# Performance work log

Hardware: AMD Instinct MI355X
Metric: run time of the kernel (lower is better)

Reference implementation:

```python
import jax, jax.numpy as jnp
import numpy as np

B, S, DM, H, DK, DH = 8, 1024, 512, 8, 32, 64
LN_EPS = 1e-5
NEG_SLOPE = 0.01  # torch LeakyReLU default


def _l2norm(t, axis=-1, eps=1e-12):
    # matches F.normalize(p=2): x / max(||x||, eps)
    n = jnp.sqrt(jnp.sum(t * t, axis=axis, keepdims=True))
    return t / jnp.maximum(n, eps)


def _layernorm(t, w, b, eps=LN_EPS):
    mu = jnp.mean(t, axis=-1, keepdims=True)
    var = jnp.mean((t - mu) ** 2, axis=-1, keepdims=True)
    return (t - mu) * jax.lax.rsqrt(var + eps) * w + b


def setup_inputs() -> dict:
    key = jax.random.key(0)
    ks = jax.random.split(key, 16)
    x = jax.random.normal(ks[0], (B, S, DM), dtype=jnp.float32)
    # causal-style mask: True = masked (upper triangle)
    attn_mask = jnp.broadcast_to(jnp.triu(jnp.ones((S, S), dtype=bool), k=1), (B, S, S))
    pairwise_dist = jax.random.uniform(ks[1], (B, S, S), dtype=jnp.float32)
    s = 0.02
    return {
        "x": x,
        "attn_mask": attn_mask,
        "pairwise_dist": pairwise_dist,
        "Wq": jax.random.normal(ks[2], (H, DK, DM), dtype=jnp.float32) * s,
        "Wk": jax.random.normal(ks[3], (H, DK, DM), dtype=jnp.float32) * s,
        "Wv": jax.random.normal(ks[4], (H, DH, DM), dtype=jnp.float32) * s,
        "omega": jnp.ones((H,), dtype=jnp.float32),
        "Wo": jax.random.normal(ks[5], (DM, H * DH), dtype=jnp.float32) * s,
        "bo": jnp.zeros((DM,), dtype=jnp.float32),
        "Wf": jax.random.normal(ks[6], (DM, DM), dtype=jnp.float32) * s,
        "bf": jnp.zeros((DM,), dtype=jnp.float32),
        "ln1_w": jnp.ones((DM,), dtype=jnp.float32),
        "ln1_b": jnp.zeros((DM,), dtype=jnp.float32),
        "ln2_w": jnp.ones((DM,), dtype=jnp.float32),
        "ln2_b": jnp.zeros((DM,), dtype=jnp.float32),
    }


def _encoder_layer(x, attn_mask, pairwise_dist, Wq, Wk, Wv, omega,
                   Wo, bo, Wf, bf, ln1_w, ln1_b, ln2_w, ln2_b):
    # --- multi-head self-attention, all heads batched ---
    q = _l2norm(jnp.einsum('bsd,hkd->hbsk', x, Wq))   # [H,B,S,DK]
    k = _l2norm(jnp.einsum('bsd,hkd->hbsk', x, Wk))
    v = jnp.einsum('bsd,hvd->hbsv', x, Wv)            # [H,B,S,DH]
    scores = jnp.einsum('hbsk,hbtk->hbst', q, k)      # cosine-sim, [H,B,S,S]
    # distance bias: exp(-omega*d) - 1, detached in the original
    r = jax.lax.stop_gradient(
        jnp.exp(-omega[:, None, None, None] * pairwise_dist[None]) - 1.0)
    scores = scores + r
    scores = jnp.where(attn_mask[None], -jnp.inf, scores)
    # custom softmax: exp(x) / (sum + 1); exp(-inf)=0 handles masking
    z = jnp.exp(scores)
    attn = z / (jnp.sum(z, axis=-1, keepdims=True) + 1.0)
    y = jnp.einsum('hbst,hbtv->hbsv', attn, v)        # [H,B,S,DH]
    y = jnp.transpose(y, (1, 2, 0, 3)).reshape(x.shape[0], x.shape[1], -1)  # concat heads
    x_attn = y @ Wo.T + bo
    # --- residual + LN + FFN (dropout p=0 -> identity) ---
    z1 = _layernorm(x + x_attn, ln1_w, ln1_b)
    z_ff = jax.nn.leaky_relu(z1 @ Wf.T + bf, negative_slope=NEG_SLOPE)
    return _layernorm(z1 + z_ff, ln2_w, ln2_b)


def reference(x, attn_mask, pairwise_dist, Wq, Wk, Wv, omega,
              Wo, bo, Wf, bf, ln1_w, ln1_b, ln2_w, ln2_b):
    return _encoder_layer(x, attn_mask, pairwise_dist, Wq, Wk, Wv, omega,
                          Wo, bo, Wf, bf, ln1_w, ln1_b, ln2_w, ln2_b)
```

## Files before the change

kernel.cpp:

```cpp
#include <hip/hip_runtime.h>
#include <hip/hip_bf16.h>
#include <math.h>
#include <stdint.h>

#define BB 8
#define SS 1024
#define DMM 512
#define HH 8
#define DKK 32
#define DHH 64

typedef __bf16 bf16x8 __attribute__((ext_vector_type(8)));
typedef float f32x4 __attribute__((ext_vector_type(4)));

__device__ __forceinline__ void gll16(const void* g, void* l) {
  __builtin_amdgcn_global_load_lds(
      (const __attribute__((address_space(1))) void*)(uintptr_t)g,
      (__attribute__((address_space(3))) void*)(uint32_t)(uintptr_t)l,
      16, 0, 0);
}

__device__ __forceinline__ uint4 pack8(const float4 a, const float4 b) {
  union { __hip_bfloat162 h2[4]; uint4 u; } p;
  p.h2[0] = __float22bfloat162_rn(make_float2(a.x, a.y));
  p.h2[1] = __float22bfloat162_rn(make_float2(a.z, a.w));
  p.h2[2] = __float22bfloat162_rn(make_float2(b.x, b.y));
  p.h2[3] = __float22bfloat162_rn(make_float2(b.z, b.w));
  return p.u;
}

__device__ __constant__ unsigned char dJ[24]  = {15,15,14,7,14,13,13,12,6,12,11,11,10,5,10,9,9,8,4,8,3,2,1,0};
__device__ __constant__ unsigned char dTB[24] = {0,8,0,0,8,0,7,0,0,7,0,6,0,0,6,0,5,0,0,5,0,0,0,0};
__device__ __constant__ unsigned char dTE[24] = {8,16,8,8,15,7,14,7,7,13,6,12,6,6,11,5,10,5,5,9,4,3,2,1};

__global__ __launch_bounds__(256) void cvt_all(
    const float* __restrict__ x, const float* __restrict__ Wq,
    const float* __restrict__ Wk, const float* __restrict__ Wv,
    const float* __restrict__ Wo, const float* __restrict__ Wf,
    __bf16* __restrict__ xb, __bf16* __restrict__ Wcat,
    __bf16* __restrict__ Wob, __bf16* __restrict__ Wfb) {
  size_t i = ((size_t)blockIdx.x * 256 + threadIdx.x) * 8;
  const float* s;
  __bf16* d;
  size_t off;
  if (i < 4194304) { s = x; d = xb + i; off = i; }
  else {
    size_t j = i - 4194304;
    if (j < 524288) {
      d = Wcat + j;
      if (j < 131072) { s = Wq; off = j; }
      else if (j < 262144) { s = Wk; off = j - 131072; }
      else { s = Wv; off = j - 262144; }
    } else {
      size_t jj = j - 524288;
      if (jj < 262144) { s = Wo; d = Wob + jj; off = jj; }
      else { s = Wf; d = Wfb + (jj - 262144); off = jj - 262144; }
    }
  }
  float4 a = *(const float4*)&s[off];
  float4 b = *(const float4*)&s[off + 4];
  *(uint4*)d = pack8(a, b);
}

__global__ __launch_bounds__(256) void gemm_qkv(
    const __bf16* __restrict__ A, const __bf16* __restrict__ W,
    __bf16* __restrict__ Qg, __bf16* __restrict__ Kg,
    __bf16* __restrict__ Vrow) {
  __shared__ __bf16 As[2][128 * 32];
  __shared__ __bf16 Bs[2][128 * 32];
  const int tid = threadIdx.x;
  const int n0 = blockIdx.x * 128;
  const int m0 = blockIdx.y * 128;
  const int lane = tid & 63;
  const int w = tid >> 6;
  const int wm = (w & 1) * 64, wn = (w >> 1) * 64;
  const int fr = lane & 15, quad = lane >> 4;
  const int srow = lane >> 2;
  const int schunk = (lane & 3) ^ ((lane >> 3) & 3);

  f32x4 acc[4][4];
#pragma unroll
  for (int mi = 0; mi < 4; ++mi)
#pragma unroll
    for (int ni = 0; ni < 4; ++ni) acc[mi][ni] = (f32x4){0.f, 0.f, 0.f, 0.f};

#pragma unroll
  for (int j = 0; j < 2; ++j) {
    const int seg = w * 2 + j;
    const int row = seg * 16 + srow;
    gll16(&A[(size_t)(m0 + row) * 512 + schunk * 8], &As[0][seg * 512]);
    gll16(&W[(size_t)(n0 + row) * 512 + schunk * 8], &Bs[0][seg * 512]);
  }
  for (int it = 0; it < 16; ++it) {
    __syncthreads();
    if (it < 15) {
      const int kt = (it + 1) * 32, ib = (it + 1) & 1;
#pragma unroll
      for (int j = 0; j < 2; ++j) {
        const int seg = w * 2 + j;
        const int row = seg * 16 + srow;
        gll16(&A[(size_t)(m0 + row) * 512 + kt + schunk * 8], &As[ib][seg * 512]);
        gll16(&W[(size_t)(n0 + row) * 512 + kt + schunk * 8], &Bs[ib][seg * 512]);
      }
    }
    const __bf16* as = As[it & 1];
    const __bf16* bs = Bs[it & 1];
    bf16x8 af[4], bfv[4];
    const int rsw = (quad ^ ((fr >> 1) & 3)) * 8;
#pragma unroll
    for (int mi = 0; mi < 4; ++mi)
      af[mi] = *(const bf16x8*)&as[(wm + mi * 16 + fr) * 32 + rsw];
#pragma unroll
    for (int ni = 0; ni < 4; ++ni)
      bfv[ni] = *(const bf16x8*)&bs[(wn + ni * 16 + fr) * 32 + rsw];
#pragma unroll
    for (int mi = 0; mi < 4; ++mi)
#pragma unroll
      for (int ni = 0; ni < 4; ++ni)
        acc[mi][ni] = __builtin_amdgcn_mfma_f32_16x16x32_bf16(
            af[mi], bfv[ni], acc[mi][ni], 0, 0, 0);
  }

  const int er = quad * 4;
  const int ec = fr;
  if (n0 < 512) {
    const bool isq = (n0 < 256);
    __bf16* G = isq ? Qg : Kg;
    const int nb = isq ? n0 : n0 - 256;
#pragma unroll
    for (int mi = 0; mi < 4; ++mi) {
#pragma unroll
      for (int p = 0; p < 2; ++p) {
        const int hh = (nb + wn + p * 32) >> 5;
#pragma unroll
        for (int r = 0; r < 4; ++r) {
          float v0 = acc[mi][2 * p][r], v1 = acc[mi][2 * p + 1][r];
          float ss = v0 * v0 + v1 * v1;
          ss += __shfl_xor(ss, 1, 64);
          ss += __shfl_xor(ss, 2, 64);
          ss += __shfl_xor(ss, 4, 64);
          ss += __shfl_xor(ss, 8, 64);
          const float sc = 1.0f / fmaxf(sqrtf(ss), 1e-12f);
          const int mm = m0 + wm + mi * 16 + er + r;
          const int bb = mm >> 10, s = mm & 1023;
          __bf16* gp = G + ((size_t)(bb * 8 + hh) * 1024 + s) * 32;
          gp[ec] = (__bf16)(v0 * sc);
          gp[16 + ec] = (__bf16)(v1 * sc);
        }
      }
    }
  } else {
#pragma unroll
    for (int mi = 0; mi < 4; ++mi)
#pragma unroll
      for (int ni = 0; ni < 4; ++ni) {
        const int n = n0 - 512 + wn + ni * 16 + ec;
#pragma unroll
        for (int r = 0; r < 4; ++r) {
          const int mm = m0 + wm + mi * 16 + er + r;
          Vrow[(size_t)mm * 512 + n] = (__bf16)acc[mi][ni][r];
        }
      }
  }
}

template <int MODE>
__global__ __launch_bounds__(256) void gemm_bf16(
    const __bf16* __restrict__ A, const __bf16* __restrict__ W,
    const float* __restrict__ bias, const float* __restrict__ resid,
    float* __restrict__ C, int N) {
  __shared__ __bf16 As[2][128 * 32];
  __shared__ __bf16 Bs[2][128 * 32];
  const int tid = threadIdx.x;
  const int n0 = blockIdx.x * 128;
  const int m0 = blockIdx.y * 128;
  const int lane = tid & 63;
  const int w = tid >> 6;
  const int wm = (w & 1) * 64, wn = (w >> 1) * 64;
  const int fr = lane & 15, quad = lane >> 4;
  const int srow = lane >> 2;
  const int schunk = (lane & 3) ^ ((lane >> 3) & 3);

  f32x4 acc[4][4];
#pragma unroll
  for (int mi = 0; mi < 4; ++mi)
#pragma unroll
    for (int ni = 0; ni < 4; ++ni) acc[mi][ni] = (f32x4){0.f, 0.f, 0.f, 0.f};

#pragma unroll
  for (int j = 0; j < 2; ++j) {
    const int seg = w * 2 + j;
    const int row = seg * 16 + srow;
    gll16(&A[(size_t)(m0 + row) * 512 + schunk * 8], &As[0][seg * 512]);
    gll16(&W[(size_t)(n0 + row) * 512 + schunk * 8], &Bs[0][seg * 512]);
  }
  for (int it = 0; it < 16; ++it) {
    __syncthreads();
    if (it < 15) {
      const int kt = (it + 1) * 32, ib = (it + 1) & 1;
#pragma unroll
      for (int j = 0; j < 2; ++j) {
        const int seg = w * 2 + j;
        const int row = seg * 16 + srow;
        gll16(&A[(size_t)(m0 + row) * 512 + kt + schunk * 8], &As[ib][seg * 512]);
        gll16(&W[(size_t)(n0 + row) * 512 + kt + schunk * 8], &Bs[ib][seg * 512]);
      }
    }
    const __bf16* as = As[it & 1];
    const __bf16* bs = Bs[it & 1];
    bf16x8 af[4], bfv[4];
    const int rsw = (quad ^ ((fr >> 1) & 3)) * 8;
#pragma unroll
    for (int mi = 0; mi < 4; ++mi)
      af[mi] = *(const bf16x8*)&as[(wm + mi * 16 + fr) * 32 + rsw];
#pragma unroll
    for (int ni = 0; ni < 4; ++ni)
      bfv[ni] = *(const bf16x8*)&bs[(wn + ni * 16 + fr) * 32 + rsw];
#pragma unroll
    for (int mi = 0; mi < 4; ++mi)
#pragma unroll
      for (int ni = 0; ni < 4; ++ni)
        acc[mi][ni] = __builtin_amdgcn_mfma_f32_16x16x32_bf16(
            af[mi], bfv[ni], acc[mi][ni], 0, 0, 0);
  }

  const int er = quad * 4;
  const int ec = fr;
#pragma unroll
  for (int mi = 0; mi < 4; ++mi) {
#pragma unroll
    for (int ni = 0; ni < 4; ++ni) {
      const int n = n0 + wn + ni * 16 + ec;
      float bsv = bias[n];
#pragma unroll
      for (int r = 0; r < 4; ++r) {
        const int m = m0 + wm + mi * 16 + er + r;
        float v = acc[mi][ni][r];
        if (MODE == 1) {
          v += bsv + resid[(size_t)m * 512 + n];
        } else {
          float g = v + bsv;
          g = g > 0.f ? g : 0.01f * g;
          v = resid[(size_t)m * 512 + n] + g;
        }
        C[(size_t)m * N + n] = v;
      }
    }
  }
}

__global__ __launch_bounds__(256) void v_transpose(
    const __bf16* __restrict__ Vrow, __bf16* __restrict__ Vt) {
  __shared__ __bf16 vt[64][136];
  const int bh = blockIdx.x;
  const int b = bh >> 3, h = bh & 7;
  const int sb = blockIdx.y * 128;
  const int tid = threadIdx.x;
#pragma unroll
  for (int i = 0; i < 8; ++i) {
    int idx = tid + i * 256;
    int t = idx >> 4, vd4 = (idx & 15) * 4;
    union { uint2 u; __bf16 e[4]; } v;
    v.u = *(const uint2*)&Vrow[((size_t)(b * 1024 + sb + t)) * 512 + h * 64 + vd4];
    vt[vd4 + 0][t] = v.e[0];
    vt[vd4 + 1][t] = v.e[1];
    vt[vd4 + 2][t] = v.e[2];
    vt[vd4 + 3][t] = v.e[3];
  }
  __syncthreads();
  {
    const int vd = tid >> 2, tseg = (tid & 3) * 32;
    uint4* o = (uint4*)(Vt + (size_t)bh * 65536 + (size_t)vd * 1024 + sb + tseg);
#pragma unroll
    for (int j = 0; j < 4; ++j)
      o[j] = *(const uint4*)&vt[vd][tseg + j * 8];
  }
}

__global__ __launch_bounds__(256) void attn_fused(
    const __bf16* __restrict__ Qg, const __bf16* __restrict__ Kg,
    const __bf16* __restrict__ Vt, const float* __restrict__ dist,
    const float* __restrict__ omega, __bf16* __restrict__ y,
    float* __restrict__ Pacc, float* __restrict__ Zb) {
  __shared__ __bf16 Ks[64 * 32];
  __shared__ __bf16 Vs[64 * 64];
  __shared__ __bf16 zbuf[4][16][72];

  const int bh = blockIdx.x;
  const int entry = blockIdx.y;
  const int b = bh >> 3, h = bh & 7;
  const int jidx = dJ[entry];
  const int tbeg = dTB[entry];
  const int tend = dTE[entry];
  const int s0 = jidx * 64;
  const int tid = threadIdx.x;
  const int lane = tid & 63;
  const int w = tid >> 6;
  const int q = lane >> 4;
  const int m = lane & 15;
  const float om = omega[h];

  const int sl = s0 + w * 16 + m;
  const bf16x8 bq = *(const bf16x8*)&Qg[((size_t)bh * 1024 + sl) * 32 + q * 8];
  const int kswz = (q ^ ((m >> 1) & 3)) * 8;

  f32x4 acc[4];
#pragma unroll
  for (int ni = 0; ni < 4; ++ni) acc[ni] = (f32x4){0.f, 0.f, 0.f, 0.f};
  float zsum = 0.0f;

  for (int tt = tbeg; tt < tend; ++tt) {
    const int t0 = tt * 64;
    __syncthreads();
    {
      int row = tid >> 2, p = tid & 3;
      uint4 v = *(const uint4*)&Kg[((size_t)bh * 1024 + t0 + row) * 32 + p * 8];
      *(uint4*)&Ks[row * 32 + ((p ^ ((row >> 1) & 3)) * 8)] = v;
    }
#pragma unroll
    for (int i = 0; i < 2; ++i) {
      int idx = tid + i * 256;
      int vd = idx >> 3, p = idx & 7;
      uint4 v = *(const uint4*)&Vt[(size_t)bh * 65536 + (size_t)vd * 1024 + t0 + p * 8];
      *(uint4*)&Vs[vd * 64 + ((p ^ (vd & 7)) * 8)] = v;
    }
    float4 dv[4];
#pragma unroll
    for (int mi = 0; mi < 4; ++mi)
      dv[mi] = *(const float4*)&dist[((size_t)b * 1024 + sl) * 1024 + t0 + 16 * mi + q * 4];
    __syncthreads();

#pragma unroll
    for (int mi = 0; mi < 4; ++mi) {
      const bf16x8 ak = *(const bf16x8*)&Ks[(16 * mi + m) * 32 + kswz];
      f32x4 s4 = __builtin_amdgcn_mfma_f32_16x16x32_bf16(
          ak, bq, (f32x4){0.f, 0.f, 0.f, 0.f}, 0, 0, 0);
      float zr[4];
#pragma unroll
      for (int r = 0; r < 4; ++r) {
        const int t = t0 + 16 * mi + q * 4 + r;
        float zv = __expf(s4[r] + __expf(-om * (&dv[mi].x)[r]) - 1.0f);
        zr[r] = (t <= sl) ? zv : 0.0f;
        zsum += zr[r];
      }
      union { __hip_bfloat162 h2[2]; uint2 u; } pz;
      pz.h2[0] = __float22bfloat162_rn(make_float2(zr[0], zr[1]));
      pz.h2[1] = __float22bfloat162_rn(make_float2(zr[2], zr[3]));
      *(uint2*)&zbuf[w][m][16 * mi + q * 4] = pz.u;
    }
    const bf16x8 az0 = *(const bf16x8*)&zbuf[w][m][q * 8];
    const bf16x8 az1 = *(const bf16x8*)&zbuf[w][m][32 + q * 8];
#pragma unroll
    for (int ni = 0; ni < 4; ++ni) {
      const bf16x8 vb0 = *(const bf16x8*)&Vs[(16 * ni + m) * 64 + ((q ^ (m & 7)) * 8)];
      const bf16x8 vb1 = *(const bf16x8*)&Vs[(16 * ni + m) * 64 + (((q + 4) ^ (m & 7)) * 8)];
      acc[ni] = __builtin_amdgcn_mfma_f32_16x16x32_bf16(az0, vb0, acc[ni], 0, 0, 0);
      acc[ni] = __builtin_amdgcn_mfma_f32_16x16x32_bf16(az1, vb1, acc[ni], 0, 0, 0);
    }
  }

  zsum += __shfl_xor(zsum, 16, 64);
  zsum += __shfl_xor(zsum, 32, 64);

  if (jidx < 8) {
#pragma unroll
    for (int r = 0; r < 4; ++r) {
      const float dn = __shfl(zsum, q * 4 + r, 64);
      const float inv = 1.0f / (dn + 1.0f);
      __bf16* yp = &y[((size_t)b * 1024 + s0 + w * 16 + q * 4 + r) * 512 + h * 64 + m];
#pragma unroll
      for (int ni = 0; ni < 4; ++ni)
        yp[ni * 16] = (__bf16)(acc[ni][r] * inv);
    }
  } else {
    const int half = (tbeg != 0) ? 1 : 0;
    const size_t pidx = (size_t)((bh * 8 + (jidx - 8)) * 2 + half);
    float* Pp = Pacc + pidx * 4096;
    float* Zp = Zb + pidx * 64;
#pragma unroll
    for (int r = 0; r < 4; ++r) {
      const int row = w * 16 + q * 4 + r;
      const float dn = __shfl(zsum, q * 4 + r, 64);
      if (m == 0) Zp[row] = dn;
#pragma unroll
      for (int ni = 0; ni < 4; ++ni)
        Pp[row * 64 + ni * 16 + m] = acc[ni][r];
    }
  }
}

__global__ __launch_bounds__(256) void attn_reduce(
    const float* __restrict__ Pacc, const float* __restrict__ Zb,
    __bf16* __restrict__ y) {
  const int e = blockIdx.x;
  const int bh = e >> 3, j = (e & 7) + 8;
  const int b = bh >> 3, h = bh & 7;
  const float* p0 = Pacc + (size_t)e * 2 * 4096;
  const float* p1 = p0 + 4096;
  const int row = threadIdx.x >> 2;
  const int c0 = (threadIdx.x & 3) * 16;
  const float z = Zb[(size_t)e * 128 + row] + Zb[(size_t)e * 128 + 64 + row];
  const float inv = 1.0f / (z + 1.0f);
  float4 o[4];
#pragma unroll
  for (int i = 0; i < 4; ++i) {
    const float4 a = *(const float4*)&p0[row * 64 + c0 + i * 4];
    const float4 c = *(const float4*)&p1[row * 64 + c0 + i * 4];
    o[i].x = (a.x + c.x) * inv; o[i].y = (a.y + c.y) * inv;
    o[i].z = (a.z + c.z) * inv; o[i].w = (a.w + c.w) * inv;
  }
  __bf16* yp = &y[((size_t)b * 1024 + j * 64 + row) * 512 + h * 64 + c0];
  *(uint4*)yp = pack8(o[0], o[1]);
  *(uint4*)(yp + 8) = pack8(o[2], o[3]);
}

__global__ __launch_bounds__(256) void ln_kernel(
    const float* __restrict__ in, const float* __restrict__ w,
    const float* __restrict__ bvec, float* __restrict__ out,
    __bf16* __restrict__ outb) {
  const int row = blockIdx.x * 4 + (threadIdx.x >> 6);
  const int lane = threadIdx.x & 63;
  const float4* ip = (const float4*)(in + (size_t)row * 512);
  float4 a = ip[lane * 2], c = ip[lane * 2 + 1];
  float s = a.x + a.y + a.z + a.w + c.x + c.y + c.z + c.w;
#pragma unroll
  for (int off = 32; off > 0; off >>= 1) s += __shfl_xor(s, off, 64);
  const float mu = s * (1.0f / 512.0f);
  a.x -= mu; a.y -= mu; a.z -= mu; a.w -= mu;
  c.x -= mu; c.y -= mu; c.z -= mu; c.w -= mu;
  float s2 = a.x * a.x + a.y * a.y + a.z * a.z + a.w * a.w +
             c.x * c.x + c.y * c.y + c.z * c.z + c.w * c.w;
#pragma unroll
  for (int off = 32; off > 0; off >>= 1) s2 += __shfl_xor(s2, off, 64);
  const float inv = rsqrtf(s2 * (1.0f / 512.0f) + 1e-5f);
  const float4 w0 = ((const float4*)w)[lane * 2], w1 = ((const float4*)w)[lane * 2 + 1];
  const float4 b0 = ((const float4*)bvec)[lane * 2], b1 = ((const float4*)bvec)[lane * 2 + 1];
  float4 o0, o1;
  o0.x = a.x * inv * w0.x + b0.x; o0.y = a.y * inv * w0.y + b0.y;
  o0.z = a.z * inv * w0.z + b0.z; o0.w = a.w * inv * w0.w + b0.w;
  o1.x = c.x * inv * w1.x + b1.x; o1.y = c.y * inv * w1.y + b1.y;
  o1.z = c.z * inv * w1.z + b1.z; o1.w = c.w * inv * w1.w + b1.w;
  float4* op = (float4*)(out + (size_t)row * 512);
  op[lane * 2] = o0; op[lane * 2 + 1] = o1;
  if (outb) *(uint4*)&outb[(size_t)row * 512 + lane * 8] = pack8(o0, o1);
}

extern "C" void kernel_launch(void* const* d_in, const int* in_sizes, int n_in,
                              void* d_out, int out_size, void* d_ws, size_t ws_size,
                              hipStream_t stream) {
  const float* x = (const float*)d_in[0];
  const float* dist = (const float*)d_in[2];
  const float* Wq = (const float*)d_in[3];
  const float* Wk = (const float*)d_in[4];
  const float* Wv = (const float*)d_in[5];
  const float* omega = (const float*)d_in[6];
  const float* Wo = (const float*)d_in[7];
  const float* bo = (const float*)d_in[8];
  const float* Wf = (const float*)d_in[9];
  const float* bf_ = (const float*)d_in[10];
  const float* ln1w = (const float*)d_in[11];
  const float* ln1b = (const float*)d_in[12];
  const float* ln2w = (const float*)d_in[13];
  const float* ln2b = (const float*)d_in[14];
  float* out = (float*)d_out;

  char* base = (char*)d_ws;
  const size_t MB = 1 << 20;
  __bf16* xb = (__bf16*)base;
  __bf16* yb = (__bf16*)base;
  __bf16* Wcat = (__bf16*)(base + 8 * MB);
  __bf16* Wob = (__bf16*)(base + 9 * MB);
  __bf16* Wfb = (__bf16*)(base + 9 * MB + 512 * 1024);
  __bf16* Qg = (__bf16*)(base + 10 * MB);
  __bf16* Kg = (__bf16*)(base + 14 * MB);
  __bf16* Vrow = (__bf16*)(base + 18 * MB);
  float* Pacc = (float*)(base + 18 * MB);
  float* t1 = (float*)(base + 18 * MB);
  __bf16* Vt = (__bf16*)(base + 34 * MB);
  __bf16* t1b = (__bf16*)(base + 34 * MB);
  float* Zb = (float*)(base + 42 * MB);

  dim3 blk(256);
  cvt_all<<<dim3(2560), blk, 0, stream>>>(x, Wq, Wk, Wv, Wo, Wf,
                                          xb, Wcat, Wob, Wfb);
  gemm_qkv<<<dim3(8, 64), blk, 0, stream>>>(xb, Wcat, Qg, Kg, Vrow);
  v_transpose<<<dim3(64, 8), blk, 0, stream>>>(Vrow, Vt);
  attn_fused<<<dim3(64, 24), blk, 0, stream>>>(Qg, Kg, Vt, dist, omega, yb,
                                               Pacc, Zb);
  attn_reduce<<<dim3(512), blk, 0, stream>>>(Pacc, Zb, yb);
  gemm_bf16<1><<<dim3(4, 64), blk, 0, stream>>>(yb, Wob, bo, x, t1, 512);
  ln_kernel<<<dim3(2048), blk, 0, stream>>>(t1, ln1w, ln1b, t1, t1b);
  gemm_bf16<2><<<dim3(4, 64), blk, 0, stream>>>(t1b, Wfb, bf_, t1, out, 512);
  ln_kernel<<<dim3(2048), blk, 0, stream>>>(out, ln2w, ln2b, out, nullptr);
}
```

Baseline: 261.4 us.

## Replace 128x128 GEMM tiles with unified 64x64 single-buffered GEMM kernel

The QKV projection and both output/FFN GEMMs move to one templated kernel using 64x64 output tiles with a BK of 64, giving 2048 or 1024 blocks instead of 512 or 256. The aim is to fill all CUs on the MI355X for these small GEMMs (M=8192, K=512). In exchange it drops the double-buffered async prefetch in favour of load, sync and compute per K step, and gets less operand reuse per block. The epilogues, including the Q/K L2 normalisation and bias/residual/LeakyReLU, are kept as mode branches.

```diff
diff --git a/kernel.cpp b/kernel.cpp
--- a/kernel.cpp
+++ b/kernel.cpp
@@ -62,188 +62,119 @@
   *(uint4*)d = pack8(a, b);
 }
 
-__global__ __launch_bounds__(256) void gemm_qkv(
+template <int MODE>
+__global__ __launch_bounds__(256) void gemm64(
     const __bf16* __restrict__ A, const __bf16* __restrict__ W,
-    __bf16* __restrict__ Qg, __bf16* __restrict__ Kg,
+    const float* __restrict__ bias, const float* __restrict__ resid,
+    float* __restrict__ C, __bf16* __restrict__ Qg, __bf16* __restrict__ Kg,
     __bf16* __restrict__ Vrow) {
-  __shared__ __bf16 As[2][128 * 32];
-  __shared__ __bf16 Bs[2][128 * 32];
+  __shared__ __bf16 As[64 * 64];
+  __shared__ __bf16 Bs[64 * 64];
   const int tid = threadIdx.x;
-  const int n0 = blockIdx.x * 128;
-  const int m0 = blockIdx.y * 128;
+  const int m0 = blockIdx.x * 64;
+  const int n0 = blockIdx.y * 64;
   const int lane = tid & 63;
   const int w = tid >> 6;
-  const int wm = (w & 1) * 64, wn = (w >> 1) * 64;
-  const int fr = lane & 15, quad = lane >> 4;
-  const int srow = lane >> 2;
-  const int schunk = (lane & 3) ^ ((lane >> 3) & 3);
-
-  f32x4 acc[4][4];
-#pragma unroll
-  for (int mi = 0; mi < 4; ++mi)
-#pragma unroll
-    for (int ni = 0; ni < 4; ++ni) acc[mi][ni] = (f32x4){0.f, 0.f, 0.f, 0.f};
-
-#pragma unroll
-  for (int j = 0; j < 2; ++j) {
-    const int seg = w * 2 + j;
-    const int row = seg * 16 + srow;
-    gll16(&A[(size_t)(m0 + row) * 512 + schunk * 8], &As[0][seg * 512]);
-    gll16(&W[(size_t)(n0 + row) * 512 + schunk * 8], &Bs[0][seg * 512]);
-  }
-  for (int it = 0; it < 16; ++it) {
+  const int wm = (w & 1) * 32, wn = (w >> 1) * 32;
+  const int fr = lane & 15, q = lane >> 4;
+  const int r8 = lane >> 3;
+  const int c8 = (lane & 7) ^ (r8 & 7);
+  const int fswz = fr & 7;
+
+  f32x4 acc[2][2];
+#pragma unroll
+  for (int mi = 0; mi < 2; ++mi)
+#pragma unroll
+    for (int ni = 0; ni < 2; ++ni) acc[mi][ni] = (f32x4){0.f, 0.f, 0.f, 0.f};
+
+  for (int kt = 0; kt < 512; kt += 64) {
     __syncthreads();
-    if (it < 15) {
-      const int kt = (it + 1) * 32, ib = (it + 1) & 1;
-#pragma unroll
-      for (int j = 0; j < 2; ++j) {
-        const int seg = w * 2 + j;
-        const int row = seg * 16 + srow;
-        gll16(&A[(size_t)(m0 + row) * 512 + kt + schunk * 8], &As[ib][seg * 512]);
-        gll16(&W[(size_t)(n0 + row) * 512 + kt + schunk * 8], &Bs[ib][seg * 512]);
-      }
-    }
-    const __bf16* as = As[it & 1];
-    const __bf16* bs = Bs[it & 1];
-    bf16x8 af[4], bfv[4];
-    const int rsw = (quad ^ ((fr >> 1) & 3)) * 8;
-#pragma unroll
-    for (int mi = 0; mi < 4; ++mi)
-      af[mi] = *(const bf16x8*)&as[(wm + mi * 16 + fr) * 32 + rsw];
-#pragma unroll
-    for (int ni = 0; ni < 4; ++ni)
-      bfv[ni] = *(const bf16x8*)&bs[(wn + ni * 16 + fr) * 32 + rsw];
-#pragma unroll
-    for (int mi = 0; mi < 4; ++mi)
-#pragma unroll
-      for (int ni = 0; ni < 4; ++ni)
-        acc[mi][ni] = __builtin_amdgcn_mfma_f32_16x16x32_bf16(
-            af[mi], bfv[ni], acc[mi][ni], 0, 0, 0);
-  }
-
-  const int er = quad * 4;
-  const int ec = fr;
-  if (n0 < 512) {
-    const bool isq = (n0 < 256);
-    __bf16* G = isq ? Qg : Kg;
-    const int nb = isq ? n0 : n0 - 256;
-#pragma unroll
-    for (int mi = 0; mi < 4; ++mi) {
-#pragma unroll
-      for (int p = 0; p < 2; ++p) {
-        const int hh = (nb + wn + p * 32) >> 5;
+#pragma unroll
+    for (int j = 0; j < 2; ++j) {
+      const int row = w * 16 + j * 8;
+      gll16(&A[(size_t)(m0 + row + r8) * 512 + kt + c8 * 8], &As[row * 64]);
+      gll16(&W[(size_t)(n0 + row + r8) * 512 + kt + c8 * 8], &Bs[row * 64]);
+    }
+    __syncthreads();
+
+    bf16x8 af[2][2], bfv[2][2];
+#pragma unroll
+    for (int ks = 0; ks < 2; ++ks) {
+#pragma unroll
+      for (int mi = 0; mi < 2; ++mi)
+        af[ks][mi] = *(const bf16x8*)&As[(wm + mi * 16 + fr) * 64 +
+                                         (((ks * 4 + q) ^ fswz) * 8)];
+#pragma unroll
+      for (int ni = 0; ni < 2; ++ni)
+        bfv[ks][ni] = *(const bf16x8*)&Bs[(wn + ni * 16 + fr) * 64 +
+                                          (((ks * 4 + q) ^ fswz) * 8)];
+    }
+#pragma unroll
+    for (int ks = 0; ks < 2; ++ks)
+#pragma unroll
+      for (int mi = 0; mi < 2; ++mi)
+#pragma unroll
+        for (int ni = 0; ni < 2; ++ni)
+          acc[mi][ni] = __builtin_amdgcn_mfma_f32_16x16x32_bf16(
+              af[ks][mi], bfv[ks][ni], acc[mi][ni], 0, 0, 0);
+  }
+
+  if (MODE == 0) {
+    if (n0 < 512) {
+      const bool isq = (n0 < 256);
+      __bf16* G = isq ? Qg : Kg;
+      const int hh = ((isq ? n0 : n0 - 256) + wn) >> 5;
+#pragma unroll
+      for (int mi = 0; mi < 2; ++mi) {
 #pragma unroll
         for (int r = 0; r < 4; ++r) {
-          float v0 = acc[mi][2 * p][r], v1 = acc[mi][2 * p + 1][r];
+          float v0 = acc[mi][0][r], v1 = acc[mi][1][r];
           float ss = v0 * v0 + v1 * v1;
           ss += __shfl_xor(ss, 1, 64);
           ss += __shfl_xor(ss, 2, 64);
           ss += __shfl_xor(ss, 4, 64);
           ss += __shfl_xor(ss, 8, 64);
           const float sc = 1.0f / fmaxf(sqrtf(ss), 1e-12f);
-          const int mm = m0 + wm + mi * 16 + er + r;
+          const int mm = m0 + wm + mi * 16 + q * 4 + r;
           const int bb = mm >> 10, s = mm & 1023;
           __bf16* gp = G + ((size_t)(bb * 8 + hh) * 1024 + s) * 32;
-          gp[ec] = (__bf16)(v0 * sc);
-          gp[16 + ec] = (__bf16)(v1 * sc);
+          gp[fr] = (__bf16)(v0 * sc);
+          gp[16 + fr] = (__bf16)(v1 * sc);
         }
       }
+    } else {
+#pragma unroll
+      for (int mi = 0; mi < 2; ++mi)
+#pragma unroll
+        for (int ni = 0; ni < 2; ++ni) {
+          const int n = n0 - 512 + wn + ni * 16 + fr;
+#pragma unroll
+          for (int r = 0; r < 4; ++r) {
+            const int mm = m0 + wm + mi * 16 + q * 4 + r;
+            Vrow[(size_t)mm * 512 + n] = (__bf16)acc[mi][ni][r];
+          }
+        }
     }
   } else {
 #pragma unroll
-    for (int mi = 0; mi < 4; ++mi)
-#pragma unroll
-      for (int ni = 0; ni < 4; ++ni) {
-        const int n = n0 - 512 + wn + ni * 16 + ec;
+    for (int mi = 0; mi < 2; ++mi) {
+#pragma unroll
+      for (int ni = 0; ni < 2; ++ni) {
+        const int n = n0 + wn + ni * 16 + fr;
+        const float bsv = bias[n];
 #pragma unroll
         for (int r = 0; r < 4; ++r) {
-          const int mm = m0 + wm + mi * 16 + er + r;
-          Vrow[(size_t)mm * 512 + n] = (__bf16)acc[mi][ni][r];
+          const int m = m0 + wm + mi * 16 + q * 4 + r;
+          float v = acc[mi][ni][r];
+          if (MODE == 1) {
+            v += bsv + resid[(size_t)m * 512 + n];
+          } else {
+            float g = v + bsv;
+            g = g > 0.f ? g : 0.01f * g;
+            v = resid[(size_t)m * 512 + n] + g;
+          }
+          C[(size_t)m * 512 + n] = v;
         }
-      }
-  }
-}
-
-template <int MODE>
-__global__ __launch_bounds__(256) void gemm_bf16(
-    const __bf16* __restrict__ A, const __bf16* __restrict__ W,
-    const float* __restrict__ bias, const float* __restrict__ resid,
-    float* __restrict__ C, int N) {
-  __shared__ __bf16 As[2][128 * 32];
-  __shared__ __bf16 Bs[2][128 * 32];
-  const int tid = threadIdx.x;
-  const int n0 = blockIdx.x * 128;
-  const int m0 = blockIdx.y * 128;
-  const int lane = tid & 63;
-  const int w = tid >> 6;
-  const int wm = (w & 1) * 64, wn = (w >> 1) * 64;
-  const int fr = lane & 15, quad = lane >> 4;
-  const int srow = lane >> 2;
-  const int schunk = (lane & 3) ^ ((lane >> 3) & 3);
-
-  f32x4 acc[4][4];
-#pragma unroll
-  for (int mi = 0; mi < 4; ++mi)
-#pragma unroll
-    for (int ni = 0; ni < 4; ++ni) acc[mi][ni] = (f32x4){0.f, 0.f, 0.f, 0.f};
-
-#pragma unroll
-  for (int j = 0; j < 2; ++j) {
-    const int seg = w * 2 + j;
-    const int row = seg * 16 + srow;
-    gll16(&A[(size_t)(m0 + row) * 512 + schunk * 8], &As[0][seg * 512]);
-    gll16(&W[(size_t)(n0 + row) * 512 + schunk * 8], &Bs[0][seg * 512]);
-  }
-  for (int it = 0; it < 16; ++it) {
-    __syncthreads();
-    if (it < 15) {
-      const int kt = (it + 1) * 32, ib = (it + 1) & 1;
-#pragma unroll
-      for (int j = 0; j < 2; ++j) {
-        const int seg = w * 2 + j;
-        const int row = seg * 16 + srow;
-        gll16(&A[(size_t)(m0 + row) * 512 + kt + schunk * 8], &As[ib][seg * 512]);
-        gll16(&W[(size_t)(n0 + row) * 512 + kt + schunk * 8], &Bs[ib][seg * 512]);
-      }
-    }
-    const __bf16* as = As[it & 1];
-    const __bf16* bs = Bs[it & 1];
-    bf16x8 af[4], bfv[4];
-    const int rsw = (quad ^ ((fr >> 1) & 3)) * 8;
-#pragma unroll
-    for (int mi = 0; mi < 4; ++mi)
-      af[mi] = *(const bf16x8*)&as[(wm + mi * 16 + fr) * 32 + rsw];
-#pragma unroll
-    for (int ni = 0; ni < 4; ++ni)
-      bfv[ni] = *(const bf16x8*)&bs[(wn + ni * 16 + fr) * 32 + rsw];
-#pragma unroll
-    for (int mi = 0; mi < 4; ++mi)
-#pragma unroll
-      for (int ni = 0; ni < 4; ++ni)
-        acc[mi][ni] = __builtin_amdgcn_mfma_f32_16x16x32_bf16(
-            af[mi], bfv[ni], acc[mi][ni], 0, 0, 0);
-  }
-
-  const int er = quad * 4;
-  const int ec = fr;
-#pragma unroll
-  for (int mi = 0; mi < 4; ++mi) {
-#pragma unroll
-    for (int ni = 0; ni < 4; ++ni) {
-      const int n = n0 + wn + ni * 16 + ec;
-      float bsv = bias[n];
-#pragma unroll
-      for (int r = 0; r < 4; ++r) {
-        const int m = m0 + wm + mi * 16 + er + r;
-        float v = acc[mi][ni][r];
-        if (MODE == 1) {
-          v += bsv + resid[(size_t)m * 512 + n];
-        } else {
-          float g = v + bsv;
-          g = g > 0.f ? g : 0.01f * g;
-          v = resid[(size_t)m * 512 + n] + g;
-        }
-        C[(size_t)m * N + n] = v;
       }
     }
   }
@@ -483,13 +414,16 @@
   dim3 blk(256);
   cvt_all<<<dim3(2560), blk, 0, stream>>>(x, Wq, Wk, Wv, Wo, Wf,
                                           xb, Wcat, Wob, Wfb);
-  gemm_qkv<<<dim3(8, 64), blk, 0, stream>>>(xb, Wcat, Qg, Kg, Vrow);
+  gemm64<0><<<dim3(128, 16), blk, 0, stream>>>(xb, Wcat, nullptr, nullptr,
+                                               nullptr, Qg, Kg, Vrow);
   v_transpose<<<dim3(64, 8), blk, 0, stream>>>(Vrow, Vt);
   attn_fused<<<dim3(64, 24), blk, 0, stream>>>(Qg, Kg, Vt, dist, omega, yb,
                                                Pacc, Zb);
   attn_reduce<<<dim3(512), blk, 0, stream>>>(Pacc, Zb, yb);
-  gemm_bf16<1><<<dim3(4, 64), blk, 0, stream>>>(yb, Wob, bo, x, t1, 512);
+  gemm64<1><<<dim3(128, 8), blk, 0, stream>>>(yb, Wob, bo, x, t1,
+                                              nullptr, nullptr, nullptr);
   ln_kernel<<<dim3(2048), blk, 0, stream>>>(t1, ln1w, ln1b, t1, t1b);
-  gemm_bf16<2><<<dim3(4, 64), blk, 0, stream>>>(t1b, Wfb, bf_, t1, out, 512);
+  gemm64<2><<<dim3(128, 8), blk, 0, stream>>>(t1b, Wfb, bf_, t1, out,
+                                              nullptr, nullptr, nullptr);
   ln_kernel<<<dim3(2048), blk, 0, stream>>>(out, ln2w, ln2b, out, nullptr);
 }
```

Result: faster. 227.7 us (-12.9%).
